# Kernel optimization log

Measured on AMD Instinct MI355X. Metric: run time of the kernel, lower is better.

## Reference

```python
import jax, jax.numpy as jnp
import numpy as np

DIM = 1024
NUM_HEADS = 16
HEAD_DIM = DIM // NUM_HEADS
B, T = 2, 2048


def setup_inputs() -> dict:
    key = jax.random.key(0)
    ks = jax.random.split(key, 7)
    x = jax.random.normal(ks[0], (B, T, DIM), dtype=jnp.float32)
    # causal mask, broadcastable over batch and heads
    mask = jnp.tril(jnp.ones((T, T), dtype=bool))[None, None, :, :]
    # rope tables for half rotary angles, tiled to head_dim (cat of two halves)
    pos = jnp.arange(T, dtype=jnp.float32)[:, None]
    inv_freq = 1.0 / (10000.0 ** (jnp.arange(0, HEAD_DIM, 2, dtype=jnp.float32) / HEAD_DIM))
    ang = pos * inv_freq[None, :]                      # [T, hd/2]
    ang = jnp.concatenate([ang, ang], axis=-1)         # [T, hd]
    rope_sin = jnp.sin(ang)[None, None, :, :]
    rope_cos = jnp.cos(ang)[None, None, :, :]
    s = 0.02
    qkv_w = jax.random.normal(ks[1], (DIM, 3 * DIM), dtype=jnp.float32) * s
    qkv_b = jnp.zeros((3 * DIM,), dtype=jnp.float32)
    proj_w = jax.random.normal(ks[2], (DIM, DIM), dtype=jnp.float32) * s
    proj_b = jnp.zeros((DIM,), dtype=jnp.float32)
    return {"x": x, "mask": mask, "rope_sin": rope_sin, "rope_cos": rope_cos,
            "qkv_w": qkv_w, "qkv_b": qkv_b, "proj_w": proj_w, "proj_b": proj_b}


def _rotate_half(t):
    half = t.shape[-1] // 2
    return jnp.concatenate([-t[..., half:], t[..., :half]], axis=-1)


def _apply_rope(t, sin, cos):
    return t * cos + _rotate_half(t) * sin


def reference(x, mask, rope_sin, rope_cos, qkv_w, qkv_b, proj_w, proj_b):
    Bb, Tt, C = x.shape
    qkv = x @ qkv_w + qkv_b                            # [B, T, 3C]
    q, k, v = jnp.split(qkv, 3, axis=-1)
    def split_heads(t):                                # [B, T, C] -> [B, H, T, hd]
        return t.reshape(Bb, Tt, NUM_HEADS, HEAD_DIM).transpose(0, 2, 1, 3)
    q, k, v = split_heads(q), split_heads(k), split_heads(v)
    sin = rope_sin[:, :, :Tt, :]
    cos = rope_cos[:, :, :Tt, :]
    q = _apply_rope(q, sin, cos)
    k = _apply_rope(k, sin, cos)
    att = jnp.einsum("bhqd,bhkd->bhqk", q, k) / (HEAD_DIM ** 0.5)
    att = jnp.where(mask, att, -jnp.inf)
    att = jax.nn.softmax(att, axis=-1)
    y = jnp.einsum("bhqk,bhkd->bhqd", att, v)          # [B, H, T, hd]
    y = y.transpose(0, 2, 1, 3).reshape(Bb, Tt, C)
    return y @ proj_w + proj_b
```

## Files before the change

kernel.cpp:

```cpp
#include <hip/hip_runtime.h>

typedef unsigned short u16;
typedef u16 u16x8 __attribute__((ext_vector_type(8)));
typedef __bf16 bf16x8 __attribute__((ext_vector_type(8)));
typedef float f32x4 __attribute__((ext_vector_type(4)));

#define T_SEQ 2048
#define DIM 1024
#define NH 16
#define HD 64

#define MFMA(a, b, c) __builtin_amdgcn_mfma_f32_16x16x32_bf16(a, b, c, 0, 0, 0)

__device__ __forceinline__ u16 f2bf(float f) {
  return __builtin_bit_cast(u16, static_cast<__bf16>(f));
}

__device__ __forceinline__ bf16x8 ld8(const u16* p) {
  return __builtin_bit_cast(bf16x8, *(const u16x8*)p);
}

__device__ __forceinline__ void gload_lds16(const u16* g, u16* l) {
  __builtin_amdgcn_global_load_lds((const __attribute__((address_space(1))) void*)(g),
                                   (__attribute__((address_space(3))) void*)(l),
                                   16, 0, 0);
}

__global__ void k_prep(const float* __restrict__ X, u16* __restrict__ Y,
                       const float* __restrict__ Wq, u16* __restrict__ WqT,
                       const float* __restrict__ Wp, u16* __restrict__ WpT) {
  __shared__ float tile[32][33];
  int bid = blockIdx.x;
  if (bid < 4096) {
    int i = (bid * 256 + threadIdx.x) * 4;
    float4 f = *(const float4*)&X[i];
    ushort4 o = make_ushort4(f2bf(f.x), f2bf(f.y), f2bf(f.z), f2bf(f.w));
    *(ushort4*)&Y[i] = o;
    return;
  }
  const float* W; u16* WT; int K = 1024, N, bx, by;
  if (bid < 4096 + 3072) { int t = bid - 4096; W = Wq; WT = WqT; N = 3072; bx = t % 96; by = t / 96; }
  else                   { int t = bid - 7168; W = Wp; WT = WpT; N = 1024; bx = t % 32; by = t / 32; }
  int tx = threadIdx.x & 31, ty = threadIdx.x >> 5;
  int c0 = bx * 32, r0 = by * 32;
#pragma unroll
  for (int r = 0; r < 4; r++)
    tile[ty + r * 8][tx] = W[(r0 + ty + r * 8) * N + c0 + tx];
  __syncthreads();
#pragma unroll
  for (int r = 0; r < 4; r++)
    WT[(c0 + ty + r * 8) * K + r0 + tx] = f2bf(tile[tx][ty + r * 8]);
}

#define GEMM_STAGE(buf, kk)                                                       \
  {                                                                               \
    _Pragma("unroll") for (int p = 0; p < 2; p++) {                               \
      int rr = w * 32 + p * 16;                                                   \
      gload_lds16(&Agp[(size_t)(rowBase + rr + srow) * Kd + (kk) + schunk],       \
                  &As[buf][rr * 32]);                                             \
      gload_lds16(&Bgp[(size_t)(colBase + rr + srow) * Kd + (kk) + schunk],       \
                  &Bs[buf][rr * 32]);                                             \
    }                                                                             \
  }

#define GEMM_COMPUTE(buf)                                                         \
  {                                                                               \
    bf16x8 af[4], bfv[4];                                                         \
    _Pragma("unroll") for (int i = 0; i < 4; i++) {                               \
      af[i] = ld8(&As[buf][(wm * 64 + i * 16 + l15) * 32 + quad * 8]);            \
      bfv[i] = ld8(&Bs[buf][(wn * 64 + i * 16 + l15) * 32 + quad * 8]);           \
    }                                                                             \
    _Pragma("unroll") for (int i = 0; i < 4; i++)                                 \
        _Pragma("unroll") for (int j = 0; j < 4; j++)                             \
            acc[i][j] = MFMA(af[i], bfv[j], acc[i][j]);                           \
  }

#define GEMM_CORE(Aptr, BTptr, Kdim, bxv, byv)                                    \
  const int tid = threadIdx.x;                                                    \
  const int lane = tid & 63, w = tid >> 6;                                        \
  const int l15 = lane & 15, quad = lane >> 4;                                    \
  const int wm = w >> 1, wn = w & 1;                                              \
  const int rowBase = (byv) * 128;                                                \
  const int colBase = (bxv) * 128;                                                \
  const u16* Agp = (Aptr);                                                        \
  const u16* Bgp = (BTptr);                                                       \
  const int Kd = (Kdim);                                                          \
  f32x4 acc[4][4];                                                                \
  _Pragma("unroll") for (int i = 0; i < 4; i++)                                   \
      _Pragma("unroll") for (int j = 0; j < 4; j++)                               \
          acc[i][j] = (f32x4){0.f, 0.f, 0.f, 0.f};                                \
  const int srow = lane >> 2;                 \
  const int schunk = (lane & 3) * 8;    \
  GEMM_STAGE(0, 0)                                                                \
  __syncthreads();                                    \
  for (int k0 = 0; k0 < Kd; k0 += 64) {                                          \
    if (k0 + 32 < Kd) GEMM_STAGE(1, k0 + 32)              \
    GEMM_COMPUTE(0)                                       \
    __syncthreads();             \
    if (k0 + 64 < Kd) GEMM_STAGE(0, k0 + 64)              \
    GEMM_COMPUTE(1)                                       \
    __syncthreads();                                                             \
  }

#define EPLD 136

__global__ __launch_bounds__(256) void k_gemm_qkv(
    const u16* __restrict__ A, const u16* __restrict__ BT,
    const float* __restrict__ bias,
    const float* __restrict__ rsin, const float* __restrict__ rcos,
    u16* __restrict__ qb, u16* __restrict__ kb, u16* __restrict__ vtb) {
  __shared__ __align__(16) u16 LDSBUF[128 * EPLD];
  u16 (*As)[128 * 32] = (u16(*)[128 * 32])(LDSBUF);
  u16 (*Bs)[128 * 32] = (u16(*)[128 * 32])(LDSBUF + 8192);
  const int n = blockIdx.x, xcd = n & 7, s = n >> 3;
  const int cg = xcd & 1, rg = xcd >> 1;
  const int bxv = cg * 12 + (s >> 3);
  const int byv = rg * 8 + (s & 7);
  GEMM_CORE(A, BT, DIM, bxv, byv)

#pragma unroll
  for (int j = 0; j < 4; j++) {
    float bv = bias[colBase + wn * 64 + j * 16 + l15];
#pragma unroll
    for (int i = 0; i < 4; i++)
#pragma unroll
      for (int r = 0; r < 4; r++) acc[i][j][r] += bv;
  }

  const int colW = colBase + wn * 64;
  const int sec = colW >> 10;

  if (sec == 2) {
#pragma unroll
    for (int i = 0; i < 4; i++)
#pragma unroll
      for (int r = 0; r < 4; r++) {
        int tl = wm * 64 + i * 16 + quad * 4 + r;
#pragma unroll
        for (int j = 0; j < 4; j++) {
          int d2 = wn * 64 + j * 16 + l15;
          LDSBUF[d2 * EPLD + tl] = f2bf(acc[i][j][r]);
        }
      }
  } else {
#pragma unroll
    for (int i = 0; i < 4; i++)
#pragma unroll
      for (int r = 0; r < 4; r++) {
        int tl = wm * 64 + i * 16 + quad * 4 + r;
        int t = (rowBase + tl) & 2047;
#pragma unroll
        for (int j = 0; j < 4; j++) {
          int d = j * 16 + l15;
          float v = acc[i][j][r];
          float pr = acc[i][j ^ 2][r];
          float rot = (j < 2) ? -pr : pr;
          float rv = v * rcos[t * HD + d] + rot * rsin[t * HD + d];
          if (sec == 0) rv *= 0.125f;
          LDSBUF[tl * EPLD + wn * 64 + d] = f2bf(rv);
        }
      }
  }
  __syncthreads();

  const int hb = (colBase & 1023) >> 6;
  const int b = rowBase >> 11, t0 = rowBase & 2047;
  if (sec == 2) {
#pragma unroll
    for (int p = 0; p < 8; p++) {
      int drow = (tid >> 4) + p * 16;
      int tc = (tid & 15) * 8;
      int hh = hb + (drow >> 6), d = drow & 63;
      u16x8 v = *(const u16x8*)&LDSBUF[drow * EPLD + tc];
      *(u16x8*)&vtb[((size_t)(b * NH + hh) * HD + d) * T_SEQ + t0 + tc] = v;
    }
  } else {
    u16* dst = (sec == 0) ? qb : kb;
#pragma unroll
    for (int p = 0; p < 8; p++) {
      int row = (tid >> 4) + p * 16;
      int dc = (tid & 15) * 8;
      int hh = hb + (dc >> 6), d = dc & 63;
      u16x8 v = *(const u16x8*)&LDSBUF[row * EPLD + dc];
      *(u16x8*)&dst[((size_t)(b * NH + hh) * T_SEQ + t0 + row) * HD + d] = v;
    }
  }
}

__global__ __launch_bounds__(256) void k_gemm_proj(
    const u16* __restrict__ A, const u16* __restrict__ BT,
    const float* __restrict__ bias, float* __restrict__ C) {
  __shared__ __align__(16) u16 LDSBUF[16384];
  u16 (*As)[128 * 32] = (u16(*)[128 * 32])(LDSBUF);
  u16 (*Bs)[128 * 32] = (u16(*)[128 * 32])(LDSBUF + 8192);
  const int n = blockIdx.x, xcd = n & 7, s = n >> 3;
  const int cg = xcd & 1, rg = xcd >> 1;
  const int bxv = cg * 4 + (s >> 3);
  const int byv = rg * 8 + (s & 7);
  GEMM_CORE(A, BT, DIM, bxv, byv)

#pragma unroll
  for (int i = 0; i < 4; i++)
#pragma unroll
    for (int r = 0; r < 4; r++) {
      int grow = rowBase + wm * 64 + i * 16 + quad * 4 + r;
#pragma unroll
      for (int j = 0; j < 4; j++) {
        int col = colBase + wn * 64 + j * 16 + l15;
        C[grow * DIM + col] = acc[i][j][r] + bias[col];
      }
    }
}

#define KLD 72
#define VLD 136

__global__ __launch_bounds__(256, 3) void k_attn(
    const u16* __restrict__ qb, const u16* __restrict__ kb,
    const u16* __restrict__ vtb, u16* __restrict__ yb) {
  __shared__ __align__(16) u16 Ks[128 * KLD];
  __shared__ __align__(16) u16 VTs[64 * VLD];
  __shared__ __align__(16) u16 Ps[64 * VLD];
  const int tid = threadIdx.x;
  const int lane = tid & 63, w = tid >> 6;
  const int l15 = lane & 15, quad = lane >> 4;
  const int bh = blockIdx.x;
  const int qt = 31 - blockIdx.y;

  const u16* qp = qb + (size_t)bh * T_SEQ * HD;
  const u16* kp = kb + (size_t)bh * T_SEQ * HD;
  const u16* vp = vtb + (size_t)bh * HD * T_SEQ;

  const int nch = (qt + 2) >> 1;
  const int qrow_base = qt * 64 + w * 16 + quad * 4;

  const int sr = tid >> 3, sc = (tid & 7) * 8;
  const int vr = tid >> 4, vc = (tid & 15) * 8;

  u16x8 kreg[4], vreg[4];
#define LOADKV(c)                                                              \
  {                                                                            \
    _Pragma("unroll") for (int p = 0; p < 4; p++)                              \
        kreg[p] = *(const u16x8*)&kp[((c) * 128 + sr + p * 32) * HD + sc];     \
    _Pragma("unroll") for (int p = 0; p < 4; p++)                              \
        vreg[p] = *(const u16x8*)&vp[(vr + p * 16) * T_SEQ + (c) * 128 + vc];  \
  }
#define WRITEKV()                                                              \
  {                                                                            \
    _Pragma("unroll") for (int p = 0; p < 4; p++)                              \
        *(u16x8*)&Ks[(sr + p * 32) * KLD + sc] = kreg[p];                      \
    _Pragma("unroll") for (int p = 0; p < 4; p++)                              \
        *(u16x8*)&VTs[(vr + p * 16) * VLD + vc] = vreg[p];                     \
  }

  LOADKV(0)

  {
#pragma unroll
    for (int p = 0; p < 2; p++) {
      int r = sr + p * 32;
      *(u16x8*)&Ps[r * KLD + sc] = *(const u16x8*)&qp[(qt * 64 + r) * HD + sc];
    }
  }
  __syncthreads();
  bf16x8 qa0 = ld8(&Ps[(w * 16 + l15) * KLD + quad * 8]);
  bf16x8 qa1 = ld8(&Ps[(w * 16 + l15) * KLD + 32 + quad * 8]);
  WRITEKV()
  __syncthreads();

  f32x4 o[4];
#pragma unroll
  for (int j = 0; j < 4; j++) o[j] = (f32x4){0.f, 0.f, 0.f, 0.f};
  float li[4] = {0.f, 0.f, 0.f, 0.f};

  u16* ps = &Ps[w * 16 * VLD];
  const int srd = ((l15 & 1) << 3) | ((l15 >> 2) << 1) | ((l15 >> 1) & 1);

  for (int c = 0; c < nch; c++) {
    if (c + 1 < nch) LOADKV(c + 1)

    f32x4 s[8];
#pragma unroll
    for (int j = 0; j < 8; j++) {
      s[j] = (f32x4){0.f, 0.f, 0.f, 0.f};
      bf16x8 b0 = ld8(&Ks[(j * 16 + l15) * KLD + quad * 8]);
      bf16x8 b1 = ld8(&Ks[(j * 16 + l15) * KLD + 32 + quad * 8]);
      s[j] = MFMA(qa0, b0, s[j]);
      s[j] = MFMA(qa1, b1, s[j]);
    }

    const bool lastc = (c == nch - 1);
#pragma unroll
    for (int r = 0; r < 4; r++) {
      const int swr = ((r & 1) << 3) | (quad << 1) | (r >> 1);
#pragma unroll
      for (int j = 0; j < 8; j++) {
        float e = __expf(s[j][r]);
        if (lastc && (c * 128 + j * 16 + l15 > qrow_base + r)) e = 0.f;
        li[r] += e;
        ps[swr * VLD + j * 16 + l15] = f2bf(e);
      }
    }

#pragma unroll
    for (int c4 = 0; c4 < 4; c4++) {
      bf16x8 pa = ld8(&ps[srd * VLD + c4 * 32 + quad * 8]);
#pragma unroll
      for (int j2 = 0; j2 < 4; j2++) {
        bf16x8 vb = ld8(&VTs[(j2 * 16 + l15) * VLD + c4 * 32 + quad * 8]);
        o[j2] = MFMA(pa, vb, o[j2]);
      }
    }
    __syncthreads();
    if (c + 1 < nch) {
      WRITEKV()
      __syncthreads();
    }
  }

#pragma unroll
  for (int r = 0; r < 4; r++) {
#pragma unroll
    for (int off = 8; off >= 1; off >>= 1) li[r] += __shfl_xor(li[r], off, 16);
    li[r] = 1.0f / li[r];
  }

#pragma unroll
  for (int j = 0; j < 4; j++)
#pragma unroll
    for (int r = 0; r < 4; r++) {
      const int swr = ((r & 1) << 3) | (quad << 1) | (r >> 1);
      ps[swr * VLD + j * 16 + l15] = f2bf(o[j][r] * li[r]);
    }
  __syncthreads();

  const int b = bh >> 4, h = bh & 15;
  {
    int sr2 = tid >> 3, sc2 = (tid & 7) * 8;
#pragma unroll
    for (int p = 0; p < 2; p++) {
      int row = sr2 + p * 32;
      int m = row & 15;
      int srow = ((m & 1) << 3) | ((m >> 2) << 1) | ((m >> 1) & 1);
      int t = qt * 64 + row;
      *(u16x8*)&yb[((size_t)(b * T_SEQ + t) * NH + h) * HD + sc2] =
          *(const u16x8*)&Ps[((row & 48) | srow) * VLD + sc2];
    }
  }
}

extern "C" void kernel_launch(void* const* d_in, const int* in_sizes, int n_in,
                              void* d_out, int out_size, void* d_ws, size_t ws_size,
                              hipStream_t stream) {
  const float* x      = (const float*)d_in[0];
  const float* rsin   = (const float*)d_in[2];
  const float* rcos   = (const float*)d_in[3];
  const float* qkv_w  = (const float*)d_in[4];
  const float* qkv_b  = (const float*)d_in[5];
  const float* proj_w = (const float*)d_in[6];
  const float* proj_b = (const float*)d_in[7];
  float* out = (float*)d_out;

  char* ws = (char*)d_ws;
  u16* x_bf  = (u16*)(ws);
  u16* qkvT  = (u16*)(ws + (8ull << 20));
  u16* projT = (u16*)(ws + (14ull << 20));
  u16* q_buf = (u16*)(ws + (16ull << 20));
  u16* k_buf = (u16*)(ws + (24ull << 20));
  u16* vT    = (u16*)(ws + (32ull << 20));
  u16* y_buf = (u16*)(ws + (40ull << 20));

  hipLaunchKernelGGL(k_prep, dim3(8192), dim3(256), 0, stream,
                     x, x_bf, qkv_w, qkvT, proj_w, projT);
  hipLaunchKernelGGL(k_gemm_qkv, dim3(768), dim3(256), 0, stream,
                     x_bf, qkvT, qkv_b, rsin, rcos, q_buf, k_buf, vT);
  hipLaunchKernelGGL(k_attn, dim3(32, 32), dim3(256), 0, stream,
                     q_buf, k_buf, vT, y_buf);
  hipLaunchKernelGGL(k_gemm_proj, dim3(256), dim3(256), 0, stream,
                     y_buf, projT, proj_b, out);
}
```

Baseline: 201.7 us.

## Keep attention probabilities in registers via shuffles and drop P LDS buffer

The attention kernel computes S transposed (K as the A operand), so each lane holds four consecutive key scores for one query. The probabilities are packed to bf16 with v_cvt_pk_bf16_f32 and rearranged into the PV MFMA operand layout with cross-lane shuffles, replacing the round trip through a shared-memory P buffer. Removing that buffer lowers LDS use enough to raise launch bounds from 3 to 4 blocks per CU. In exchange it adds many shuffle and select instructions per chunk plus one extra barrier when Q staging reuses the K buffer.

```diff
diff --git a/kernel.cpp b/kernel.cpp
--- a/kernel.cpp
+++ b/kernel.cpp
@@ -2,6 +2,7 @@
 
 typedef unsigned short u16;
 typedef u16 u16x8 __attribute__((ext_vector_type(8)));
+typedef unsigned u32x4 __attribute__((ext_vector_type(4)));
 typedef __bf16 bf16x8 __attribute__((ext_vector_type(8)));
 typedef float f32x4 __attribute__((ext_vector_type(4)));
 
@@ -215,12 +216,11 @@
 #define KLD 72
 #define VLD 136
 
-__global__ __launch_bounds__(256, 3) void k_attn(
+__global__ __launch_bounds__(256, 4) void k_attn(
     const u16* __restrict__ qb, const u16* __restrict__ kb,
     const u16* __restrict__ vtb, u16* __restrict__ yb) {
   __shared__ __align__(16) u16 Ks[128 * KLD];
   __shared__ __align__(16) u16 VTs[64 * VLD];
-  __shared__ __align__(16) u16 Ps[64 * VLD];
   const int tid = threadIdx.x;
   const int lane = tid & 63, w = tid >> 6;
   const int l15 = lane & 15, quad = lane >> 4;
@@ -232,7 +232,9 @@
   const u16* vp = vtb + (size_t)bh * HD * T_SEQ;
 
   const int nch = (qt + 2) >> 1;
-  const int qrow_base = qt * 64 + w * 16 + quad * 4;
+  const int qg = qt * 64 + w * 16 + l15;
+
+  const f32x4 zf4 = {0.f, 0.f, 0.f, 0.f};
 
   const int sr = tid >> 3, sc = (tid & 7) * 8;
   const int vr = tid >> 4, vc = (tid & 15) * 8;
@@ -259,22 +261,24 @@
 #pragma unroll
     for (int p = 0; p < 2; p++) {
       int r = sr + p * 32;
-      *(u16x8*)&Ps[r * KLD + sc] = *(const u16x8*)&qp[(qt * 64 + r) * HD + sc];
-    }
-  }
-  __syncthreads();
-  bf16x8 qa0 = ld8(&Ps[(w * 16 + l15) * KLD + quad * 8]);
-  bf16x8 qa1 = ld8(&Ps[(w * 16 + l15) * KLD + 32 + quad * 8]);
+      *(u16x8*)&Ks[r * KLD + sc] = *(const u16x8*)&qp[(qt * 64 + r) * HD + sc];
+    }
+  }
+  __syncthreads();
+  bf16x8 qa0 = ld8(&Ks[(w * 16 + l15) * KLD + quad * 8]);
+  bf16x8 qa1 = ld8(&Ks[(w * 16 + l15) * KLD + 32 + quad * 8]);
+  __syncthreads();
   WRITEKV()
   __syncthreads();
 
   f32x4 o[4];
 #pragma unroll
-  for (int j = 0; j < 4; j++) o[j] = (f32x4){0.f, 0.f, 0.f, 0.f};
-  float li[4] = {0.f, 0.f, 0.f, 0.f};
-
-  u16* ps = &Ps[w * 16 * VLD];
-  const int srd = ((l15 & 1) << 3) | ((l15 >> 2) << 1) | ((l15 >> 1) & 1);
+  for (int j = 0; j < 4; j++) o[j] = zf4;
+  float li = 0.f;
+
+  const int srcl0 = l15 + ((quad & 1) << 5);
+  const int srcl1 = srcl0 + 16;
+  const bool hiq = (quad >> 1) != 0;
 
   for (int c = 0; c < nch; c++) {
     if (c + 1 < nch) LOADKV(c + 1)
@@ -282,29 +286,48 @@
     f32x4 s[8];
 #pragma unroll
     for (int j = 0; j < 8; j++) {
-      s[j] = (f32x4){0.f, 0.f, 0.f, 0.f};
-      bf16x8 b0 = ld8(&Ks[(j * 16 + l15) * KLD + quad * 8]);
-      bf16x8 b1 = ld8(&Ks[(j * 16 + l15) * KLD + 32 + quad * 8]);
-      s[j] = MFMA(qa0, b0, s[j]);
-      s[j] = MFMA(qa1, b1, s[j]);
-    }
-
+      bf16x8 k0 = ld8(&Ks[(j * 16 + l15) * KLD + quad * 8]);
+      bf16x8 k1 = ld8(&Ks[(j * 16 + l15) * KLD + 32 + quad * 8]);
+      s[j] = MFMA(k0, qa0, zf4);
+      s[j] = MFMA(k1, qa1, s[j]);
+    }
+
+    unsigned ulo[8], uhi[8];
     const bool lastc = (c == nch - 1);
-#pragma unroll
-    for (int r = 0; r < 4; r++) {
-      const int swr = ((r & 1) << 3) | (quad << 1) | (r >> 1);
-#pragma unroll
-      for (int j = 0; j < 8; j++) {
-        float e = __expf(s[j][r]);
-        if (lastc && (c * 128 + j * 16 + l15 > qrow_base + r)) e = 0.f;
-        li[r] += e;
-        ps[swr * VLD + j * 16 + l15] = f2bf(e);
-      }
+    const int kb0 = c * 128 + quad * 4;
+#pragma unroll
+    for (int j = 0; j < 8; j++) {
+      float e[4];
+#pragma unroll
+      for (int r = 0; r < 4; r++) {
+        float ev = __expf(s[j][r]);
+        if (lastc && (kb0 + j * 16 + r > qg)) ev = 0.f;
+        li += ev;
+        e[r] = ev;
+      }
+      asm("v_cvt_pk_bf16_f32 %0, %1, %2" : "=v"(ulo[j]) : "v"(e[0]), "v"(e[1]));
+      asm("v_cvt_pk_bf16_f32 %0, %1, %2" : "=v"(uhi[j]) : "v"(e[2]), "v"(e[3]));
     }
 
 #pragma unroll
     for (int c4 = 0; c4 < 4; c4++) {
-      bf16x8 pa = ld8(&ps[srd * VLD + c4 * 32 + quad * 8]);
+      unsigned a0 = ulo[2 * c4], b0 = ulo[2 * c4 + 1];
+      unsigned a1 = uhi[2 * c4], b1 = uhi[2 * c4 + 1];
+      unsigned xa, xb;
+      xa = (unsigned)__shfl((int)a0, srcl0, 64);
+      xb = (unsigned)__shfl((int)b0, srcl0, 64);
+      unsigned w0 = hiq ? xb : xa;
+      xa = (unsigned)__shfl((int)a1, srcl0, 64);
+      xb = (unsigned)__shfl((int)b1, srcl0, 64);
+      unsigned w1 = hiq ? xb : xa;
+      xa = (unsigned)__shfl((int)a0, srcl1, 64);
+      xb = (unsigned)__shfl((int)b0, srcl1, 64);
+      unsigned w2 = hiq ? xb : xa;
+      xa = (unsigned)__shfl((int)a1, srcl1, 64);
+      xb = (unsigned)__shfl((int)b1, srcl1, 64);
+      unsigned w3 = hiq ? xb : xa;
+      u32x4 pw = {w0, w1, w2, w3};
+      bf16x8 pa = __builtin_bit_cast(bf16x8, pw);
 #pragma unroll
       for (int j2 = 0; j2 < 4; j2++) {
         bf16x8 vb = ld8(&VTs[(j2 * 16 + l15) * VLD + c4 * 32 + quad * 8]);
@@ -318,34 +341,28 @@
     }
   }
 
-#pragma unroll
-  for (int r = 0; r < 4; r++) {
-#pragma unroll
-    for (int off = 8; off >= 1; off >>= 1) li[r] += __shfl_xor(li[r], off, 16);
-    li[r] = 1.0f / li[r];
-  }
+  li += __shfl_xor(li, 16, 64);
+  li += __shfl_xor(li, 32, 64);
+  float inv = 1.0f / li;
+  float invr[4];
+#pragma unroll
+  for (int r = 0; r < 4; r++)
+    invr[r] = __shfl(inv, (lane & 48) | (quad * 4 + r), 64);
 
 #pragma unroll
   for (int j = 0; j < 4; j++)
 #pragma unroll
-    for (int r = 0; r < 4; r++) {
-      const int swr = ((r & 1) << 3) | (quad << 1) | (r >> 1);
-      ps[swr * VLD + j * 16 + l15] = f2bf(o[j][r] * li[r]);
-    }
+    for (int r = 0; r < 4; r++)
+      Ks[(w * 16 + quad * 4 + r) * KLD + j * 16 + l15] = f2bf(o[j][r] * invr[r]);
   __syncthreads();
 
   const int b = bh >> 4, h = bh & 15;
-  {
-    int sr2 = tid >> 3, sc2 = (tid & 7) * 8;
-#pragma unroll
-    for (int p = 0; p < 2; p++) {
-      int row = sr2 + p * 32;
-      int m = row & 15;
-      int srow = ((m & 1) << 3) | ((m >> 2) << 1) | ((m >> 1) & 1);
-      int t = qt * 64 + row;
-      *(u16x8*)&yb[((size_t)(b * T_SEQ + t) * NH + h) * HD + sc2] =
-          *(const u16x8*)&Ps[((row & 48) | srow) * VLD + sc2];
-    }
+#pragma unroll
+  for (int p = 0; p < 2; p++) {
+    int row = sr + p * 32;
+    int t = qt * 64 + row;
+    *(u16x8*)&yb[((size_t)(b * T_SEQ + t) * NH + h) * HD + sc] =
+        *(const u16x8*)&Ks[row * KLD + sc];
   }
 }
 
```

After: 216.9 us. 1.08x slower.

## Triple-buffer GEMM K-loop with vmcnt waits and a single barrier per step

Applied to the files above, without the earlier changes.

Replaces the double-buffered GEMM main loop in the QKV and projection kernels with a fully unrolled triple-buffered pipeline over 32-wide K steps. Each step waits with a partial vmcnt so the prefetch two stages ahead stays in flight, then issues one barrier instead of two. This is meant to hide global-to-LDS load latency better and cut barrier count. It raises LDS use to 48KB per block, which may lower occupancy, and full unrolling increases code size.

```diff
diff --git a/kernel.cpp b/kernel.cpp
--- a/kernel.cpp
+++ b/kernel.cpp
@@ -52,7 +52,8 @@
     WT[(c0 + ty + r * 8) * K + r0 + tx] = f2bf(tile[tx][ty + r * 8]);
 }
 
-#define GEMM_STAGE(buf, kk)                                                       \
+
+#define GEMM_STAGE3(buf, kk)                                                      \
   {                                                                               \
     _Pragma("unroll") for (int p = 0; p < 2; p++) {                               \
       int rr = w * 32 + p * 16;                                                   \
@@ -63,7 +64,7 @@
     }                                                                             \
   }
 
-#define GEMM_COMPUTE(buf)                                                         \
+#define GEMM_COMPUTE3(buf)                                                        \
   {                                                                               \
     bf16x8 af[4], bfv[4];                                                         \
     _Pragma("unroll") for (int i = 0; i < 4; i++) {                               \
@@ -75,7 +76,7 @@
             acc[i][j] = MFMA(af[i], bfv[j], acc[i][j]);                           \
   }
 
-#define GEMM_CORE(Aptr, BTptr, Kdim, bxv, byv)                                    \
+#define GEMM_CORE3(Aptr, BTptr, bxv, byv)                                         \
   const int tid = threadIdx.x;                                                    \
   const int lane = tid & 63, w = tid >> 6;                                        \
   const int l15 = lane & 15, quad = lane >> 4;                                    \
@@ -84,23 +85,23 @@
   const int colBase = (bxv) * 128;                                                \
   const u16* Agp = (Aptr);                                                        \
   const u16* Bgp = (BTptr);                                                       \
-  const int Kd = (Kdim);                                                          \
+  const int Kd = DIM;                                                             \
   f32x4 acc[4][4];                                                                \
   _Pragma("unroll") for (int i = 0; i < 4; i++)                                   \
       _Pragma("unroll") for (int j = 0; j < 4; j++)                               \
           acc[i][j] = (f32x4){0.f, 0.f, 0.f, 0.f};                                \
   const int srow = lane >> 2;                 \
   const int schunk = (lane & 3) * 8;    \
-  GEMM_STAGE(0, 0)                                                                \
-  __syncthreads();                                    \
-  for (int k0 = 0; k0 < Kd; k0 += 64) {                                          \
-    if (k0 + 32 < Kd) GEMM_STAGE(1, k0 + 32)              \
-    GEMM_COMPUTE(0)                                       \
-    __syncthreads();             \
-    if (k0 + 64 < Kd) GEMM_STAGE(0, k0 + 64)              \
-    GEMM_COMPUTE(1)                                       \
-    __syncthreads();                                                             \
-  }
+  GEMM_STAGE3(0, 0)                                                               \
+  GEMM_STAGE3(1, 32)                                                              \
+  _Pragma("unroll") for (int s = 0; s < 32; ++s) {                                \
+    if (s < 31) { asm volatile("s_waitcnt vmcnt(4)" ::: "memory"); }              \
+    else        { asm volatile("s_waitcnt vmcnt(0)" ::: "memory"); }              \
+    __builtin_amdgcn_s_barrier();                                                 \
+    if (s + 2 < 32) { GEMM_STAGE3((s + 2) % 3, (s + 2) * 32) }                    \
+    GEMM_COMPUTE3(s % 3)                                                          \
+  }                                                                               \
+  __syncthreads();
 
 #define EPLD 136
 
@@ -109,14 +110,14 @@
     const float* __restrict__ bias,
     const float* __restrict__ rsin, const float* __restrict__ rcos,
     u16* __restrict__ qb, u16* __restrict__ kb, u16* __restrict__ vtb) {
-  __shared__ __align__(16) u16 LDSBUF[128 * EPLD];
+  __shared__ __align__(16) u16 LDSBUF[24576];
   u16 (*As)[128 * 32] = (u16(*)[128 * 32])(LDSBUF);
-  u16 (*Bs)[128 * 32] = (u16(*)[128 * 32])(LDSBUF + 8192);
+  u16 (*Bs)[128 * 32] = (u16(*)[128 * 32])(LDSBUF + 12288);
   const int n = blockIdx.x, xcd = n & 7, s = n >> 3;
   const int cg = xcd & 1, rg = xcd >> 1;
   const int bxv = cg * 12 + (s >> 3);
   const int byv = rg * 8 + (s & 7);
-  GEMM_CORE(A, BT, DIM, bxv, byv)
+  GEMM_CORE3(A, BT, bxv, byv)
 
 #pragma unroll
   for (int j = 0; j < 4; j++) {
@@ -190,14 +191,14 @@
 __global__ __launch_bounds__(256) void k_gemm_proj(
     const u16* __restrict__ A, const u16* __restrict__ BT,
     const float* __restrict__ bias, float* __restrict__ C) {
-  __shared__ __align__(16) u16 LDSBUF[16384];
+  __shared__ __align__(16) u16 LDSBUF[24576];
   u16 (*As)[128 * 32] = (u16(*)[128 * 32])(LDSBUF);
-  u16 (*Bs)[128 * 32] = (u16(*)[128 * 32])(LDSBUF + 8192);
+  u16 (*Bs)[128 * 32] = (u16(*)[128 * 32])(LDSBUF + 12288);
   const int n = blockIdx.x, xcd = n & 7, s = n >> 3;
   const int cg = xcd & 1, rg = xcd >> 1;
   const int bxv = cg * 4 + (s >> 3);
   const int byv = rg * 8 + (s & 7);
-  GEMM_CORE(A, BT, DIM, bxv, byv)
+  GEMM_CORE3(A, BT, bxv, byv)
 
 #pragma unroll
   for (int i = 0; i < 4; i++)
```

Result: faster. 188.2 us (-6.7%).
